# Optimization experiments

Hardware: AMD Instinct MI355X
Metric: run time of the kernel (lower is better)

## Reference

```python
import jax, jax.numpy as jnp
import numpy as np

LMAX, MMAX, C = 4, 2, 128
E, N = 40000, 4000
CUTOFF, RESCALE = 12.0, 5.0
EPS = 1e-5

def _mappings(lmax, mmax):
    # l-major coefficient listing with m in [-min(l,mmax), min(l,mmax)]
    m_list = []
    for l in range(lmax + 1):
        mm = min(l, mmax)
        m_list += list(range(-mm, mm + 1))
    m_c = np.array(m_list)
    n = len(m_list)
    to_m = np.zeros((n, n), dtype=np.float32)  # m-major <- l-major permutation
    off = 0
    for m in range(mmax + 1):
        idx_r = np.where(m_c == m)[0]
        for i, j in enumerate(idx_r):
            to_m[off + i, j] = 1.0
        off += len(idx_r)
        if m > 0:
            idx_i = np.where(m_c == -m)[0]
            for i, j in enumerate(idx_i):
                to_m[off + i, j] = 1.0
            off += len(idx_i)
    full_m = np.concatenate([np.arange(-l, l + 1) for l in range(lmax + 1)])
    out_idx = np.where(np.abs(full_m) <= mmax)[0]  # out_mask as index list
    return jnp.asarray(to_m), jnp.asarray(out_idx)

TO_M, OUT_IDX = _mappings(LMAX, MMAX)
M0 = LMAX + 1            # number of m=0 coefficients (5)
M_ALL = TO_M.shape[0]    # number of |m|<=mmax coefficients (19)
NCOEF = (LMAX + 1) ** 2  # full coefficient count (25)

def setup_inputs() -> dict:
    key = jax.random.key(0)
    ks = jax.random.split(key, 8)
    return {
        "x": jax.random.normal(ks[0], (N, NCOEF, C), jnp.float32),
        "x_edge": jax.random.normal(ks[1], (E, 128), jnp.float32),
        "edge_distance": jax.random.uniform(ks[2], (E,), jnp.float32) * CUTOFF,
        "wigner_inv": jax.random.normal(ks[3], (E, NCOEF, NCOEF), jnp.float32) / np.float32(np.sqrt(NCOEF)),
        "edge_index": jax.random.randint(ks[4], (2, E), 0, N),
        "w1": jax.random.normal(ks[5], (128, 64), jnp.float32) / np.float32(np.sqrt(128.0)),
        "b1": jnp.zeros((64,), jnp.float32),
        "g1": jnp.ones((64,), jnp.float32),
        "be1": jnp.zeros((64,), jnp.float32),
        "w2": jax.random.normal(ks[6], (64, 64), jnp.float32) / 8.0,
        "b2": jnp.zeros((64,), jnp.float32),
        "g2": jnp.ones((64,), jnp.float32),
        "be2": jnp.zeros((64,), jnp.float32),
        "w3": jax.random.normal(ks[7], (64, M0 * C), jnp.float32) / 8.0,
        "b3": jnp.zeros((M0 * C,), jnp.float32),
        "node_offset": 0,
    }

def _ln(h, g, b):
    mu = jnp.mean(h, -1, keepdims=True)
    var = jnp.mean((h - mu) ** 2, -1, keepdims=True)
    return (h - mu) * jax.lax.rsqrt(var + EPS) * g + b

def _envelope(d):
    # PolynomialEnvelope with exponent p=5
    p = 5.0
    a = -(p + 1.0) * (p + 2.0) / 2.0   # -21
    bb = p * (p + 2.0)                 #  35
    c = -p * (p + 1.0) / 2.0           # -15
    env = 1.0 + a * d**5 + bb * d**6 + c * d**7
    return jnp.where(d < 1.0, env, jnp.zeros_like(d))

def reference(x, x_edge, edge_distance, wigner_inv, edge_index,
              w1, b1, g1, be1, w2, b2, g2, be2, w3, b3, node_offset):
    # RadialMLP: (Linear -> LayerNorm -> SiLU) x2 -> Linear
    h = jax.nn.silu(_ln(x_edge @ w1 + b1, g1, be1))
    h = jax.nn.silu(_ln(h @ w2 + b2, g2, be2))
    m0 = (h @ w3 + b3).reshape(-1, M0, C)               # [E, M0, C]
    # zero-padding to M_ALL rows then applying the permutation TO_M equals
    # contracting only the first M0 (m=0) rows of TO_M
    emb = jnp.einsum("nac,ab->nbc", m0, TO_M[:M0])       # [E, M_ALL, C] (l-order)
    emb = jnp.einsum("nij,njc->nic", wigner_inv[:, :, OUT_IDX], emb)  # [E, NCOEF, C]
    env = _envelope(edge_distance / CUTOFF)
    emb = emb * env[:, None, None]
    dst = edge_index[1] - node_offset
    return x.at[dst].add(emb / RESCALE)
```

## Files before the change

kernel.cpp:

```cpp
#include <hip/hip_runtime.h>
#include <cstddef>


constexpr int C_DIM   = 128;
constexpr int NCOEF   = 25;
constexpr int M0d     = 5;
constexpr int MCH     = 4;
constexpr float EPS_LN      = 1e-5f;
constexpr float INV_CUTOFF  = 1.0f / 12.0f;
constexpr float INV_RESCALE = 0.2f;

typedef __attribute__((ext_vector_type(8))) short short8;
typedef __attribute__((ext_vector_type(4))) short short4v;
typedef __attribute__((ext_vector_type(4))) float f32x4;

__device__ __forceinline__ short f2bf(float f) {
    unsigned u = __float_as_uint(f);
    unsigned r = u + 0x7FFFu + ((u >> 16) & 1u);
    return (short)(r >> 16);
}

__device__ __forceinline__ float silu(float z) {
    return z / (1.0f + __expf(-z));
}

__global__ __launch_bounds__(256) void zero_kernel(int* __restrict__ p, int n) {
    int i = blockIdx.x * 256 + threadIdx.x;
    if (i < n) p[i] = 0;
}

__global__ __launch_bounds__(256) void prep_weights(
    const float* __restrict__ w1, const float* __restrict__ w2,
    const float* __restrict__ w3,
    short* __restrict__ w1T, short* __restrict__ w2T, short* __restrict__ w3T)
{
    int i = blockIdx.x * 256 + threadIdx.x;
    if (i < 64 * 128) {
        int n = i >> 7, k = i & 127;
        w1T[i] = f2bf(w1[k * 64 + n]);
    }
    if (i < 64 * 64) {
        int n = i >> 6, k = i & 63;
        w2T[i] = f2bf(w2[k * 64 + n]);
    }
    if (i < 640 * 64) {
        int n = i >> 6, k = i & 63;
        w3T[i] = f2bf(w3[k * 640 + n]);
    }
}

__global__ __launch_bounds__(256) void count_kernel(
    const int* __restrict__ edge_index, const int* __restrict__ noff,
    int* __restrict__ cnt, int E, int N)
{
    int e = blockIdx.x * 256 + threadIdx.x;
    if (e < E) {
        int d = edge_index[E + e] - noff[0];
        if (d >= 0 && d < N) atomicAdd(&cnt[d], 1);
    }
}

__global__ __launch_bounds__(256) void scan_kernel(
    const int* __restrict__ cnt, int* __restrict__ offs, int N)
{
    __shared__ int s_wsum[4];
    const int t = threadIdx.x;
    const int lane = t & 63, w = t >> 6;
    const int chunk = (N + 255) / 256;
    const int base = t * chunk;

    int s = 0;
    for (int j = 0; j < chunk; ++j)
        if (base + j < N) s += cnt[base + j];

    int v = s;
    #pragma unroll
    for (int off = 1; off < 64; off <<= 1) {
        int u = __shfl_up(v, off, 64);
        if (lane >= off) v += u;
    }
    if (lane == 63) s_wsum[w] = v;
    __syncthreads();
    int wbase = 0;
    for (int k = 0; k < w; ++k) wbase += s_wsum[k];
    int run = wbase + v - s;

    if (t == 0) offs[0] = 0;
    for (int j = 0; j < chunk; ++j) {
        if (base + j < N) {
            run += cnt[base + j];
            offs[base + j + 1] = run;
        }
    }
}

__global__ __launch_bounds__(256) void fill_kernel(
    const int* __restrict__ edge_index, const int* __restrict__ noff,
    const int* __restrict__ offs, int* __restrict__ cur,
    int* __restrict__ ipos, int E, int N)
{
    int e = blockIdx.x * 256 + threadIdx.x;
    if (e < E) {
        int d = edge_index[E + e] - noff[0];
        if (d >= 0 && d < N) {
            int p = atomicAdd(&cur[d], 1);
            ipos[e] = offs[d] + p;
        }
    }
}

__global__ __launch_bounds__(256) void compact_kernel(
    const float* __restrict__ wigner_inv,
    const int*   __restrict__ ipos,
    unsigned short* __restrict__ wkT,
    int E)
{
    __shared__ float s_raw[16 * 625];
    __shared__ int   s_ipos[16];

    const int t  = threadIdx.x;
    const int g0 = blockIdx.x * 16;
    const int nloc = (E - g0) < 16 ? (E - g0) : 16;

    if (t < nloc) s_ipos[t] = ipos[g0 + t];

    if (nloc == 16) {
        const float4* src = (const float4*)(wigner_inv + (size_t)g0 * 625);
        #pragma unroll 4
        for (int f = t; f < 2500; f += 256)
            *(float4*)&s_raw[f * 4] = src[f];
    } else {
        const float* src = wigner_inv + (size_t)g0 * 625;
        for (int f = t; f < nloc * 625; f += 256)
            s_raw[f] = src[f];
    }
    __syncthreads();

    const int total = nloc * 160;
    #pragma unroll 4
    for (int f = t; f < total; f += 256) {
        int el = f / 160;
        int r  = f - el * 160;
        int a  = r >> 5;
        int i  = r & 31;
        int ip = s_ipos[el];
        if ((unsigned)ip < (unsigned)E) {
            unsigned short v = 0;
            if (i < 25) v = (unsigned short)f2bf(s_raw[el * 625 + i * 25 + a * (a + 1)]);
            wkT[((size_t)ip * 5 + a) * 32 + i] = v;
        }
    }
}

__global__ __launch_bounds__(256, 2) void mlp_mfma_kernel(
    const float* __restrict__ x_edge,
    const float* __restrict__ edge_distance,
    const int*   __restrict__ ipos,
    const short* __restrict__ w1T,
    const float* __restrict__ b1,
    const float* __restrict__ g1, const float* __restrict__ be1,
    const short* __restrict__ w2T,
    const float* __restrict__ b2,
    const float* __restrict__ g2, const float* __restrict__ be2,
    const short* __restrict__ w3T,
    const float* __restrict__ b3,
    unsigned short* __restrict__ m0p,
    int E, int nChunk)
{
    __shared__ float s_part[128];
    __shared__ short sh1[1024];
    __shared__ short sh2[1024];

    const int t   = threadIdx.x;
    const int w   = t >> 6;
    const int l   = t & 63;
    const int e16 = l & 15;
    const int g   = l >> 4;
    const int swz = (e16 & 7) << 4;

    char* sh1b = (char*)sh1;
    char* sh2b = (char*)sh2;

    short8 aw1[4], aw2[2], aw3a[10], aw3b[10];
    #pragma unroll
    for (int kt = 0; kt < 4; ++kt)
        aw1[kt] = *(const short8*)(w1T + (w * 16 + e16) * 128 + kt * 32 + 8 * g);
    #pragma unroll
    for (int kt = 0; kt < 2; ++kt)
        aw2[kt] = *(const short8*)(w2T + (w * 16 + e16) * 64 + kt * 32 + 8 * g);
    #pragma unroll
    for (int j = 0; j < 10; ++j) {
        const int nt = w * 10 + j;
        aw3a[j] = *(const short8*)(w3T + (nt * 16 + e16) * 64 + 8 * g);
        aw3b[j] = *(const short8*)(w3T + (nt * 16 + e16) * 64 + 32 + 8 * g);
    }
    const float4 b1v  = *(const float4*)(b1  + w * 16 + 4 * g);
    const float4 g1v  = *(const float4*)(g1  + w * 16 + 4 * g);
    const float4 be1v = *(const float4*)(be1 + w * 16 + 4 * g);
    const float4 b2v  = *(const float4*)(b2  + w * 16 + 4 * g);
    const float4 g2v  = *(const float4*)(g2  + w * 16 + 4 * g);
    const float4 be2v = *(const float4*)(be2 + w * 16 + 4 * g);
    float4 b3v[10];
    #pragma unroll
    for (int j = 0; j < 10; ++j)
        b3v[j] = *(const float4*)(b3 + (w * 10 + j) * 16 + 4 * g);

    const int ch0 = (int)blockIdx.x * MCH;
    const int chE = (ch0 + MCH < nChunk) ? (ch0 + MCH) : nChunk;

    for (int ch = ch0; ch < chE; ++ch) {
        const int g0  = ch * 16;
        const int row = g0 + e16;
        const int rowc = row < E ? row : (E - 1);
        const bool valid = row < E;

        float sc;
        {
            float d  = edge_distance[rowc] * INV_CUTOFF;
            float d2 = d * d;
            float d5 = d2 * d2 * d;
            float env = 1.0f + d5 * (-21.0f + d * (35.0f + d * (-15.0f)));
            sc = ((d < 1.0f) ? env : 0.0f) * INV_RESCALE;
        }
        const int ip = valid ? ipos[rowc] : 0;
        const bool ipok = valid && ((unsigned)ip < (unsigned)E);

        short8 bx[4];
        {
            const float* xr = x_edge + (size_t)rowc * C_DIM + 8 * g;
            #pragma unroll
            for (int kt = 0; kt < 4; ++kt) {
                float4 f0 = *(const float4*)(xr + kt * 32);
                float4 f1 = *(const float4*)(xr + kt * 32 + 4);
                short8 v;
                v[0] = f2bf(f0.x); v[1] = f2bf(f0.y); v[2] = f2bf(f0.z); v[3] = f2bf(f0.w);
                v[4] = f2bf(f1.x); v[5] = f2bf(f1.y); v[6] = f2bf(f1.z); v[7] = f2bf(f1.w);
                bx[kt] = v;
            }
        }

        f32x4 acc1 = {b1v.x, b1v.y, b1v.z, b1v.w};
        #pragma unroll
        for (int kt = 0; kt < 4; ++kt)
            acc1 = __builtin_amdgcn_mfma_f32_16x16x32_bf16(aw1[kt], bx[kt], acc1, 0, 0, 0);

        {
            float s = acc1[0] + acc1[1] + acc1[2] + acc1[3];
            s += __shfl_xor(s, 16);
            s += __shfl_xor(s, 32);
            if (g == 0) s_part[w * 16 + e16] = s;
            __syncthreads();
            float mu = (s_part[e16] + s_part[16 + e16] + s_part[32 + e16] + s_part[48 + e16])
                       * (1.0f / 64.0f);
            float q = 0.0f;
            #pragma unroll
            for (int r = 0; r < 4; ++r) { float d = acc1[r] - mu; q += d * d; }
            q += __shfl_xor(q, 16);
            q += __shfl_xor(q, 32);
            if (g == 0) s_part[64 + w * 16 + e16] = q;
            __syncthreads();
            float qt = s_part[64 + e16] + s_part[80 + e16] + s_part[96 + e16] + s_part[112 + e16];
            float rstd = rsqrtf(qt * (1.0f / 64.0f) + EPS_LN);
            short4v hv;
            hv[0] = f2bf(silu((acc1[0] - mu) * rstd * g1v.x + be1v.x));
            hv[1] = f2bf(silu((acc1[1] - mu) * rstd * g1v.y + be1v.y));
            hv[2] = f2bf(silu((acc1[2] - mu) * rstd * g1v.z + be1v.z));
            hv[3] = f2bf(silu((acc1[3] - mu) * rstd * g1v.w + be1v.w));
            *(short4v*)(sh1b + e16 * 128 + ((w * 32 + 8 * g) ^ swz)) = hv;
            __syncthreads();
        }

        f32x4 acc2 = {b2v.x, b2v.y, b2v.z, b2v.w};
        {
            short8 bh[2];
            #pragma unroll
            for (int kt = 0; kt < 2; ++kt)
                bh[kt] = *(const short8*)(sh1b + e16 * 128 + ((kt * 64 + 16 * g) ^ swz));
            #pragma unroll
            for (int kt = 0; kt < 2; ++kt)
                acc2 = __builtin_amdgcn_mfma_f32_16x16x32_bf16(aw2[kt], bh[kt], acc2, 0, 0, 0);
        }

        {
            float s = acc2[0] + acc2[1] + acc2[2] + acc2[3];
            s += __shfl_xor(s, 16);
            s += __shfl_xor(s, 32);
            if (g == 0) s_part[w * 16 + e16] = s;
            __syncthreads();
            float mu = (s_part[e16] + s_part[16 + e16] + s_part[32 + e16] + s_part[48 + e16])
                       * (1.0f / 64.0f);
            float q = 0.0f;
            #pragma unroll
            for (int r = 0; r < 4; ++r) { float d = acc2[r] - mu; q += d * d; }
            q += __shfl_xor(q, 16);
            q += __shfl_xor(q, 32);
            if (g == 0) s_part[64 + w * 16 + e16] = q;
            __syncthreads();
            float qt = s_part[64 + e16] + s_part[80 + e16] + s_part[96 + e16] + s_part[112 + e16];
            float rstd = rsqrtf(qt * (1.0f / 64.0f) + EPS_LN);
            short4v hv;
            hv[0] = f2bf(silu((acc2[0] - mu) * rstd * g2v.x + be2v.x));
            hv[1] = f2bf(silu((acc2[1] - mu) * rstd * g2v.y + be2v.y));
            hv[2] = f2bf(silu((acc2[2] - mu) * rstd * g2v.z + be2v.z));
            hv[3] = f2bf(silu((acc2[3] - mu) * rstd * g2v.w + be2v.w));
            *(short4v*)(sh2b + e16 * 128 + ((w * 32 + 8 * g) ^ swz)) = hv;
            __syncthreads();
        }

        {
            short8 bh2[2];
            #pragma unroll
            for (int kt = 0; kt < 2; ++kt)
                bh2[kt] = *(const short8*)(sh2b + e16 * 128 + ((kt * 64 + 16 * g) ^ swz));

            #pragma unroll
            for (int j = 0; j < 10; ++j) {
                const int nt = w * 10 + j;
                f32x4 a3 = {b3v[j].x, b3v[j].y, b3v[j].z, b3v[j].w};
                a3 = __builtin_amdgcn_mfma_f32_16x16x32_bf16(aw3a[j], bh2[0], a3, 0, 0, 0);
                a3 = __builtin_amdgcn_mfma_f32_16x16x32_bf16(aw3b[j], bh2[1], a3, 0, 0, 0);
                if (ipok) {
                    short4v o;
                    o[0] = f2bf(a3[0] * sc);
                    o[1] = f2bf(a3[1] * sc);
                    o[2] = f2bf(a3[2] * sc);
                    o[3] = f2bf(a3[3] * sc);
                    *(short4v*)(m0p + ((size_t)ip * 5 + (nt >> 3)) * 128
                                    + ((nt & 7) << 4) + 4 * g) = o;
                }
            }
        }
        __syncthreads();
    }
}

__global__ __launch_bounds__(256, 4) void gather_mfma_kernel(
    const float* __restrict__ x,
    const unsigned short* __restrict__ m0p,
    const unsigned short* __restrict__ wkT,
    const int* __restrict__ offs,
    float* __restrict__ out, int N)
{
    const int n  = blockIdx.x;
    const int t  = threadIdx.x;
    const int w  = t >> 6;
    const int l  = t & 63;
    const int ln = l & 15;
    const int q  = l >> 4;
    const int myk = 8 * q;

    const int beg = offs[n], end = offs[n + 1];
    const int K = 5 * (end - beg);
    const size_t beg5 = (size_t)5 * beg;
    const size_t obase = (size_t)n * (NCOEF * C_DIM);

    float xv[2][4][2];
    #pragma unroll
    for (int mt = 0; mt < 2; ++mt) {
        #pragma unroll
        for (int r = 0; r < 4; ++r) {
            const int i = mt * 16 + 4 * q + r;
            #pragma unroll
            for (int bt = 0; bt < 2; ++bt)
                xv[mt][r][bt] = (i < NCOEF)
                    ? x[obase + (size_t)i * C_DIM + 32 * w + bt * 16 + ln] : 0.0f;
        }
    }

    f32x4 acc[2][2];
    #pragma unroll
    for (int mt = 0; mt < 2; ++mt)
        #pragma unroll
        for (int bt = 0; bt < 2; ++bt)
            acc[mt][bt] = (f32x4){0.f, 0.f, 0.f, 0.f};

    const int nk = (K + 31) >> 5;

#define LOADF(KT, AF, BF) do {                                                  \
    const int kb_ = (KT) * 32;                                                  \
    const int limit_ = K - kb_;                                                 \
    const unsigned short* wrow_ = wkT + (beg5 + kb_ + myk) * 32 + ln;           \
    const unsigned short* mrow_ = m0p + (beg5 + kb_ + myk) * 128 + w * 32 + ln; \
    _Pragma("unroll")                                                           \
    for (int j = 0; j < 8; ++j) {                                               \
        const bool ok_ = (myk + j) < limit_;                                    \
        AF[0][j] = ok_ ? (short)wrow_[j * 32] : (short)0;                       \
        AF[1][j] = ok_ ? (short)wrow_[j * 32 + 16] : (short)0;                  \
        BF[0][j] = ok_ ? (short)mrow_[j * 128] : (short)0;                      \
        BF[1][j] = ok_ ? (short)mrow_[j * 128 + 16] : (short)0;                 \
    } } while (0)

#define MFMA4(AF, BF) do {                                                              \
    acc[0][0] = __builtin_amdgcn_mfma_f32_16x16x32_bf16(AF[0], BF[0], acc[0][0], 0,0,0);\
    acc[0][1] = __builtin_amdgcn_mfma_f32_16x16x32_bf16(AF[0], BF[1], acc[0][1], 0,0,0);\
    acc[1][0] = __builtin_amdgcn_mfma_f32_16x16x32_bf16(AF[1], BF[0], acc[1][0], 0,0,0);\
    acc[1][1] = __builtin_amdgcn_mfma_f32_16x16x32_bf16(AF[1], BF[1], acc[1][1], 0,0,0);\
    } while (0)

    short8 afA[2], bfA[2], afB[2], bfB[2];
    if (nk > 0) {
        LOADF(0, afA, bfA);
        int kt = 0;
        while (true) {
            if (kt + 1 < nk) LOADF(kt + 1, afB, bfB);
            MFMA4(afA, bfA);
            ++kt;
            if (kt >= nk) break;
            if (kt + 1 < nk) LOADF(kt + 1, afA, bfA);
            MFMA4(afB, bfB);
            ++kt;
            if (kt >= nk) break;
        }
    }
#undef LOADF
#undef MFMA4

    #pragma unroll
    for (int mt = 0; mt < 2; ++mt) {
        #pragma unroll
        for (int r = 0; r < 4; ++r) {
            const int i = mt * 16 + 4 * q + r;
            if (i < NCOEF) {
                #pragma unroll
                for (int bt = 0; bt < 2; ++bt) {
                    const size_t idx = obase + (size_t)i * C_DIM + 32 * w + bt * 16 + ln;
                    out[idx] = xv[mt][r][bt] + acc[mt][bt][r];
                }
            }
        }
    }
}

constexpr int FEB = 8;
constexpr int BT  = 256;

__device__ __forceinline__ float ln_silu(float v, float g, float be) {
    float s = v;
    #pragma unroll
    for (int o = 32; o; o >>= 1) s += __shfl_xor(s, o, 64);
    float mu = s * (1.0f / 64.0f);
    float dv = v - mu;
    float q  = dv * dv;
    #pragma unroll
    for (int o = 32; o; o >>= 1) q += __shfl_xor(q, o, 64);
    float rstd = rsqrtf(q * (1.0f / 64.0f) + EPS_LN);
    float z = dv * rstd * g + be;
    return z / (1.0f + __expf(-z));
}

__global__ __launch_bounds__(BT) void edge_degree_fallback(
    const float* __restrict__ x_edge, const float* __restrict__ edge_distance,
    const float* __restrict__ wigner_inv, const int* __restrict__ edge_index,
    const float* __restrict__ w1, const float* __restrict__ b1,
    const float* __restrict__ g1, const float* __restrict__ be1,
    const float* __restrict__ w2, const float* __restrict__ b2,
    const float* __restrict__ g2, const float* __restrict__ be2,
    const float* __restrict__ w3, const float* __restrict__ b3,
    const int* __restrict__ node_offset_p, float* __restrict__ out, int E)
{
    __shared__ float s_xe[FEB][C_DIM];
    __shared__ float s_h1[FEB][64];
    __shared__ float s_h2[FEB][64];
    __shared__ float s_wig[FEB][NCOEF * M0d];
    __shared__ float s_scale[FEB];
    __shared__ int   s_dst[FEB];

    const int t = threadIdx.x;
    const int g0 = blockIdx.x * FEB;
    const int ne = (E - g0) < FEB ? (E - g0) : FEB;

    {
        const float* src = x_edge + (size_t)g0 * C_DIM;
        for (int f = t; f < FEB * C_DIM; f += BT) {
            int e = f >> 7;
            ((float*)s_xe)[f] = (e < ne) ? src[f] : 0.0f;
        }
    }
    {
        const int wcol_[M0d] = {0, 2, 6, 12, 20};
        for (int f = t; f < FEB * NCOEF * M0d; f += BT) {
            int e = f / 125, r = f - e * 125, i = r / 5, a = r - i * 5;
            float v = 0.0f;
            if (e < ne)
                v = wigner_inv[((size_t)(g0 + e)) * (NCOEF * NCOEF) + i * NCOEF + wcol_[a]];
            s_wig[e][r] = v;
        }
    }
    if (t < FEB) {
        if (t < ne) {
            float d = edge_distance[g0 + t] * INV_CUTOFF;
            float d2 = d * d, d5 = d2 * d2 * d;
            float env = 1.0f + d5 * (-21.0f + d * (35.0f + d * (-15.0f)));
            s_scale[t] = ((d < 1.0f) ? env : 0.0f) * INV_RESCALE;
            s_dst[t] = edge_index[E + g0 + t] - node_offset_p[0];
        } else { s_scale[t] = 0.0f; s_dst[t] = 0; }
    }
    __syncthreads();

    const int wv = t >> 6, j = t & 63;
    {
        float acc0 = b1[j], acc1 = acc0;
        for (int k = 0; k < C_DIM; ++k) {
            float w = w1[k * 64 + j];
            acc0 += s_xe[wv][k] * w;
            acc1 += s_xe[wv + 4][k] * w;
        }
        const float g = g1[j], be = be1[j];
        s_h1[wv][j]     = ln_silu(acc0, g, be);
        s_h1[wv + 4][j] = ln_silu(acc1, g, be);
    }
    __syncthreads();
    {
        float acc0 = b2[j], acc1 = acc0;
        for (int k = 0; k < 64; ++k) {
            float w = w2[k * 64 + j];
            acc0 += s_h1[wv][k] * w;
            acc1 += s_h1[wv + 4][k] * w;
        }
        const float g = g2[j], be = be2[j];
        s_h2[wv][j]     = ln_silu(acc0, g, be);
        s_h2[wv + 4][j] = ln_silu(acc1, g, be);
    }
    __syncthreads();

    const int c = t & 127, half = t >> 7;
    float m0r[4][M0d];
    #pragma unroll
    for (int a = 0; a < M0d; ++a) {
        float bb = b3[a * C_DIM + c];
        float a0 = bb, a1 = bb, a2 = bb, a3 = bb;
        const float* w3c = w3 + a * C_DIM + c;
        for (int k = 0; k < 64; ++k) {
            float w = w3c[k * (M0d * C_DIM)];
            a0 += s_h2[half + 0][k] * w;
            a1 += s_h2[half + 2][k] * w;
            a2 += s_h2[half + 4][k] * w;
            a3 += s_h2[half + 6][k] * w;
        }
        m0r[0][a] = a0; m0r[1][a] = a1; m0r[2][a] = a2; m0r[3][a] = a3;
    }
    #pragma unroll
    for (int ei = 0; ei < 4; ++ei) {
        const int e = half + 2 * ei;
        if (e >= ne) continue;
        const float sc = s_scale[e];
        float* obase = out + (size_t)s_dst[e] * (NCOEF * C_DIM) + c;
        #pragma unroll
        for (int i = 0; i < NCOEF; ++i) {
            const float* wg = &s_wig[e][i * M0d];
            float v = wg[0] * m0r[ei][0] + wg[1] * m0r[ei][1] + wg[2] * m0r[ei][2]
                    + wg[3] * m0r[ei][3] + wg[4] * m0r[ei][4];
            atomicAdd(obase + i * C_DIM, v * sc);
        }
    }
}

extern "C" void kernel_launch(void* const* d_in, const int* in_sizes, int n_in,
                              void* d_out, int out_size, void* d_ws, size_t ws_size,
                              hipStream_t stream)
{
    const float* x             = (const float*)d_in[0];
    const float* x_edge        = (const float*)d_in[1];
    const float* edge_distance = (const float*)d_in[2];
    const float* wigner_inv    = (const float*)d_in[3];
    const int*   edge_index    = (const int*)d_in[4];
    const float* w1  = (const float*)d_in[5];
    const float* b1  = (const float*)d_in[6];
    const float* g1  = (const float*)d_in[7];
    const float* be1 = (const float*)d_in[8];
    const float* w2  = (const float*)d_in[9];
    const float* b2  = (const float*)d_in[10];
    const float* g2  = (const float*)d_in[11];
    const float* be2 = (const float*)d_in[12];
    const float* w3  = (const float*)d_in[13];
    const float* b3  = (const float*)d_in[14];
    const int*   node_offset = (const int*)d_in[15];

    float* out = (float*)d_out;
    const int E = in_sizes[1] / C_DIM;
    const int N = in_sizes[0] / (NCOEF * C_DIM);
    const size_t KROWS = (size_t)5 * E + 32;

    size_t off = 0;
    const size_t m0p_off  = off; off += KROWS * 128 * 2;
    const size_t wkT_off  = off; off += KROWS * 32 * 2;
    const size_t cnt_off  = off; off += (size_t)N * 4;
    const size_t cur_off  = off; off += (size_t)N * 4;
    const size_t offs_off = off; off += (size_t)(N + 1) * 4;
    const size_t ipos_off = off; off += (size_t)E * 4;
    off = (off + 255) & ~(size_t)255;
    const size_t w1T_off  = off; off += 64 * 128 * 2;
    const size_t w2T_off  = off; off += 64 * 64 * 2;
    const size_t w3T_off  = off; off += 640 * 64 * 2;
    const size_t need     = off;

    if (ws_size >= need) {
        char* ws   = (char*)d_ws;
        unsigned short* m0p = (unsigned short*)(ws + m0p_off);
        unsigned short* wkT = (unsigned short*)(ws + wkT_off);
        int* cnt   = (int*)(ws + cnt_off);
        int* cur   = (int*)(ws + cur_off);
        int* offs  = (int*)(ws + offs_off);
        int* ipos  = (int*)(ws + ipos_off);
        short* w1T = (short*)(ws + w1T_off);
        short* w2T = (short*)(ws + w2T_off);
        short* w3T = (short*)(ws + w3T_off);

        zero_kernel<<<(2 * N + 255) / 256, 256, 0, stream>>>(cnt, 2 * N);
        prep_weights<<<(640 * 64 + 255) / 256, 256, 0, stream>>>(w1, w2, w3, w1T, w2T, w3T);
        count_kernel<<<(E + 255) / 256, 256, 0, stream>>>(edge_index, node_offset, cnt, E, N);
        scan_kernel<<<1, 256, 0, stream>>>(cnt, offs, N);
        fill_kernel<<<(E + 255) / 256, 256, 0, stream>>>(edge_index, node_offset, offs, cur, ipos, E, N);

        compact_kernel<<<(E + 15) / 16, 256, 0, stream>>>(wigner_inv, ipos, wkT, E);

        const int nChunk = (E + 15) / 16;
        mlp_mfma_kernel<<<(nChunk + MCH - 1) / MCH, 256, 0, stream>>>(
            x_edge, edge_distance, ipos,
            w1T, b1, g1, be1, w2T, b2, g2, be2, w3T, b3, m0p, E, nChunk);

        gather_mfma_kernel<<<N, 256, 0, stream>>>(x, m0p, wkT, offs, out, N);
    } else {
        hipMemcpyAsync(out, x, (size_t)out_size * sizeof(float),
                       hipMemcpyDeviceToDevice, stream);
        edge_degree_fallback<<<(E + FEB - 1) / FEB, BT, 0, stream>>>(
            x_edge, edge_distance, wigner_inv, edge_index,
            w1, b1, g1, be1, w2, b2, g2, be2, w3, b3,
            node_offset, out, E);
    }
}
```

Measured before the change: 131.3 us.

## Merge wigner compaction and radial MLP into one interleaved launch

```diff
diff --git a/kernel.cpp b/kernel.cpp
--- a/kernel.cpp
+++ b/kernel.cpp
@@ -109,52 +109,10 @@
     }
 }
 
-__global__ __launch_bounds__(256) void compact_kernel(
-    const float* __restrict__ wigner_inv,
-    const int*   __restrict__ ipos,
-    unsigned short* __restrict__ wkT,
-    int E)
-{
-    __shared__ float s_raw[16 * 625];
-    __shared__ int   s_ipos[16];
-
-    const int t  = threadIdx.x;
-    const int g0 = blockIdx.x * 16;
-    const int nloc = (E - g0) < 16 ? (E - g0) : 16;
-
-    if (t < nloc) s_ipos[t] = ipos[g0 + t];
-
-    if (nloc == 16) {
-        const float4* src = (const float4*)(wigner_inv + (size_t)g0 * 625);
-        #pragma unroll 4
-        for (int f = t; f < 2500; f += 256)
-            *(float4*)&s_raw[f * 4] = src[f];
-    } else {
-        const float* src = wigner_inv + (size_t)g0 * 625;
-        for (int f = t; f < nloc * 625; f += 256)
-            s_raw[f] = src[f];
-    }
-    __syncthreads();
-
-    const int total = nloc * 160;
-    #pragma unroll 4
-    for (int f = t; f < total; f += 256) {
-        int el = f / 160;
-        int r  = f - el * 160;
-        int a  = r >> 5;
-        int i  = r & 31;
-        int ip = s_ipos[el];
-        if ((unsigned)ip < (unsigned)E) {
-            unsigned short v = 0;
-            if (i < 25) v = (unsigned short)f2bf(s_raw[el * 625 + i * 25 + a * (a + 1)]);
-            wkT[((size_t)ip * 5 + a) * 32 + i] = v;
-        }
-    }
-}
-
-__global__ __launch_bounds__(256, 2) void mlp_mfma_kernel(
+__global__ __launch_bounds__(256, 2) void mlp_compact_kernel(
     const float* __restrict__ x_edge,
     const float* __restrict__ edge_distance,
+    const float* __restrict__ wigner_inv,
     const int*   __restrict__ ipos,
     const short* __restrict__ w1T,
     const float* __restrict__ b1,
@@ -165,21 +123,63 @@
     const short* __restrict__ w3T,
     const float* __restrict__ b3,
     unsigned short* __restrict__ m0p,
-    int E, int nChunk)
-{
-    __shared__ float s_part[128];
-    __shared__ short sh1[1024];
-    __shared__ short sh2[1024];
-
-    const int t   = threadIdx.x;
+    unsigned short* __restrict__ wkT,
+    int E, int nChunk, int nMlpBlk, int nCptBlk)
+{
+    __shared__ __align__(16) char smem[40064];
+    const int t = threadIdx.x;
+    const int group = (int)blockIdx.x / 5;
+    const int sub   = (int)blockIdx.x - group * 5;
+
+    if (sub != 0) {
+        const int cb = group * 4 + (sub - 1);
+        if (cb >= nCptBlk) return;
+        float* s_raw = (float*)smem;
+        int*   s_ipos = (int*)(smem + 40000);
+
+        const int g0 = cb * 16;
+        const int nloc = (E - g0) < 16 ? (E - g0) : 16;
+        if (t < nloc) s_ipos[t] = ipos[g0 + t];
+
+        if (nloc == 16) {
+            const float4* src = (const float4*)(wigner_inv + (size_t)g0 * 625);
+            #pragma unroll 4
+            for (int f = t; f < 2500; f += 256)
+                *(float4*)&s_raw[f * 4] = src[f];
+        } else {
+            const float* src = wigner_inv + (size_t)g0 * 625;
+            for (int f = t; f < nloc * 625; f += 256)
+                s_raw[f] = src[f];
+        }
+        __syncthreads();
+
+        const int total = nloc * 160;
+        #pragma unroll 4
+        for (int f = t; f < total; f += 256) {
+            int el = f / 160;
+            int r  = f - el * 160;
+            int a  = r >> 5;
+            int i  = r & 31;
+            int ip = s_ipos[el];
+            if ((unsigned)ip < (unsigned)E) {
+                unsigned short v = 0;
+                if (i < 25) v = (unsigned short)f2bf(s_raw[el * 625 + i * 25 + a * (a + 1)]);
+                wkT[((size_t)ip * 5 + a) * 32 + i] = v;
+            }
+        }
+        return;
+    }
+
+    if (group >= nMlpBlk) return;
+    float* s_part = (float*)smem;
+    char*  sh1b   = smem + 512;
+    char*  sh2b   = smem + 512 + 2048;
+
     const int w   = t >> 6;
     const int l   = t & 63;
     const int e16 = l & 15;
     const int g   = l >> 4;
     const int swz = (e16 & 7) << 4;
-
-    char* sh1b = (char*)sh1;
-    char* sh2b = (char*)sh2;
 
     short8 aw1[4], aw2[2], aw3a[10], aw3b[10];
     #pragma unroll
@@ -205,12 +205,12 @@
     for (int j = 0; j < 10; ++j)
         b3v[j] = *(const float4*)(b3 + (w * 10 + j) * 16 + 4 * g);
 
-    const int ch0 = (int)blockIdx.x * MCH;
+    const int ch0 = group * MCH;
     const int chE = (ch0 + MCH < nChunk) ? (ch0 + MCH) : nChunk;
 
     for (int ch = ch0; ch < chE; ++ch) {
-        const int g0  = ch * 16;
-        const int row = g0 + e16;
+        const int eg0 = ch * 16;
+        const int row = eg0 + e16;
         const int rowc = row < E ? row : (E - 1);
         const bool valid = row < E;
 
@@ -612,12 +612,14 @@
         scan_kernel<<<1, 256, 0, stream>>>(cnt, offs, N);
         fill_kernel<<<(E + 255) / 256, 256, 0, stream>>>(edge_index, node_offset, offs, cur, ipos, E, N);
 
-        compact_kernel<<<(E + 15) / 16, 256, 0, stream>>>(wigner_inv, ipos, wkT, E);
-
-        const int nChunk = (E + 15) / 16;
-        mlp_mfma_kernel<<<(nChunk + MCH - 1) / MCH, 256, 0, stream>>>(
-            x_edge, edge_distance, ipos,
-            w1T, b1, g1, be1, w2T, b2, g2, be2, w3T, b3, m0p, E, nChunk);
+        const int nChunk  = (E + 15) / 16;
+        const int nMlpBlk = (nChunk + MCH - 1) / MCH;
+        const int nCptBlk = nChunk;
+        const int nGroups = nMlpBlk > (nCptBlk + 3) / 4 ? nMlpBlk : (nCptBlk + 3) / 4;
+        mlp_compact_kernel<<<nGroups * 5, 256, 0, stream>>>(
+            x_edge, edge_distance, wigner_inv, ipos,
+            w1T, b1, g1, be1, w2T, b2, g2, be2, w3T, b3,
+            m0p, wkT, E, nChunk, nMlpBlk, nCptBlk);
 
         gather_mfma_kernel<<<N, 256, 0, stream>>>(x, m0p, wkT, offs, out, N);
     } else {
```

Result: slower. 134.8 us (+2.7%).
